# Kernel optimization log

Measured on AMD Instinct MI355X. Metric: run time of the kernel, lower is better.

The kernel has to match this reference:

```python
import jax, jax.numpy as jnp
import numpy as np


def silu(x):
    return x * jax.nn.sigmoid(x)


def setup_inputs() -> dict:
    key = jax.random.key(0)
    ks = jax.random.split(key, 9)
    d_model, d_inner, d_state, d_conv, dt_rank = 1024, 2048, 16, 4, 64
    B, L = 2, 1024
    s = 0.02  # weight init scale for numerical sanity
    return {
        "hidden_states": jax.random.normal(ks[0], (B, L, d_model), jnp.float32),
        "in_proj_w": jax.random.normal(ks[1], (2 * d_inner, d_model), jnp.float32) * s,
        "conv_w": jax.random.normal(ks[2], (d_inner, 1, d_conv), jnp.float32) * 0.2,
        "conv_b": jax.random.normal(ks[3], (d_inner,), jnp.float32) * 0.1,
        "x_proj_w": jax.random.normal(ks[4], (dt_rank + 2 * d_state, d_inner), jnp.float32) * s,
        "dt_proj_w": jax.random.normal(ks[5], (d_inner, dt_rank), jnp.float32) * (dt_rank ** -0.5),
        "dt_proj_b": jax.random.normal(ks[6], (d_inner,), jnp.float32) - 4.0,  # small dt like real init
        "A_log": jnp.log(jnp.tile(jnp.arange(1.0, d_state + 1.0, dtype=jnp.float32)[None, :], (d_inner, 1))),
        "D": jnp.ones((d_inner,), jnp.float32),
        "out_proj_w": jax.random.normal(ks[7], (d_model, d_inner), jnp.float32) * s,
    }


def reference(hidden_states, in_proj_w, conv_w, conv_b, x_proj_w,
              dt_proj_w, dt_proj_b, A_log, D, out_proj_w):
    Bsz, L, _ = hidden_states.shape
    d_inner, d_state = A_log.shape
    dt_rank = dt_proj_w.shape[1]
    K = conv_w.shape[-1]

    xz = jnp.einsum('bld,ed->ble', hidden_states, in_proj_w)  # (B,L,2*di)
    x, z = xz[..., :d_inner], xz[..., d_inner:]

    # causal depthwise conv1d (torch pads K-1 both sides then trims to L)
    xp = jnp.pad(x, ((0, 0), (K - 1, 0), (0, 0)))  # left-pad (B, L+K-1, di)
    w = conv_w[:, 0, :]  # (di, K)
    x = sum(xp[:, k:k + L, :] * w[:, k] for k in range(K)) + conv_b
    x = silu(x)

    x_dbl = jnp.einsum('bld,ed->ble', x, x_proj_w)  # (B,L,dt_rank+2n)
    dt = x_dbl[..., :dt_rank]
    Bm = x_dbl[..., dt_rank:dt_rank + d_state]
    Cm = x_dbl[..., dt_rank + d_state:]
    dt = jax.nn.softplus(jnp.einsum('blr,dr->bld', dt, dt_proj_w) + dt_proj_b)

    A = -jnp.exp(A_log)  # (di, n)
    deltaA = jnp.exp(jnp.einsum('bld,dn->bldn', dt, A))        # (B,L,di,n)
    deltaB_u = jnp.einsum('bld,bln,bld->bldn', dt, Bm, x)      # (B,L,di,n)

    def step(h, inp):
        dA_t, dBu_t, c_t = inp                # (B,di,n),(B,di,n),(B,n)
        h = dA_t * h + dBu_t
        y_t = jnp.einsum('bdn,bn->bd', h, c_t)
        return h, y_t

    h0 = jnp.zeros((Bsz, d_inner, d_state), deltaA.dtype)
    _, ys = jax.lax.scan(step, h0, (deltaA.transpose(1, 0, 2, 3),
                                    deltaB_u.transpose(1, 0, 2, 3),
                                    Cm.transpose(1, 0, 2)))
    y = ys.transpose(1, 0, 2) + x * D        # (B,L,di)
    y = y * silu(z)
    return jnp.einsum('bld,ed->ble', y, out_proj_w)
```

## Files before the change

kernel.cpp:

```cpp
#include <hip/hip_runtime.h>

typedef unsigned short u16;
typedef unsigned int   u32;
typedef __attribute__((ext_vector_type(8))) short bf16x8;
typedef __attribute__((ext_vector_type(4))) float f32x4;

__device__ inline float bf2f(u16 u) { return __uint_as_float(((u32)u) << 16); }
__device__ inline u16 f2bf(float f) {
  u32 u = __float_as_uint(f);
  return (u16)((u + 0x7FFFu + ((u >> 16) & 1u)) >> 16);
}

__device__ inline void gld_lds16(const u16* g, u16* l) {
  __builtin_amdgcn_global_load_lds((const __attribute__((address_space(1))) void*)g,
                                   (__attribute__((address_space(3))) void*)l,
                                   16, 0, 0);
}

__global__ __launch_bounds__(256) void cvt_k(
    const float* __restrict__ hs, const float* __restrict__ w_in,
    const float* __restrict__ w_x, const float* __restrict__ w_dt,
    const float* __restrict__ w_out,
    u16* __restrict__ hs_b, u16* __restrict__ w_in_b, u16* __restrict__ w_x_b,
    u16* __restrict__ w_dt_b, u16* __restrict__ w_out_b)
{
  u32 v = blockIdx.x * 256 + threadIdx.x;
  const float* s; u16* d; u32 loc;
  if      (v < 524288u)  { s = hs;    d = hs_b;    loc = v; }
  else if (v < 1572864u) { s = w_in;  d = w_in_b;  loc = v - 524288u; }
  else if (v < 1622016u) { s = w_x;   d = w_x_b;   loc = v - 1572864u; }
  else if (v < 1654784u) { s = w_dt;  d = w_dt_b;  loc = v - 1622016u; }
  else                   { s = w_out; d = w_out_b; loc = v - 1654784u; }
  float4 f = ((const float4*)s)[loc];
  ushort4 o;
  o.x = f2bf(f.x); o.y = f2bf(f.y); o.z = f2bf(f.z); o.w = f2bf(f.w);
  ((ushort4*)d)[loc] = o;
}

template <int EPI>
__global__ __launch_bounds__(256) void gemm_bt(
    const u16* __restrict__ A, int lda,
    const u16* __restrict__ B, int ldb,
    void* __restrict__ C, int ldc,
    int M, int N, int K,
    const float* __restrict__ bias)
{
  __shared__ u16 sA[128 * 32];
  __shared__ u16 sB[128 * 32];
  const int tid  = threadIdx.x;
  const int wave = tid >> 6, lane = tid & 63;
  const int row0 = blockIdx.x * 128, col0 = blockIdx.y * 128;
  const int r  = lane >> 2, c8 = (lane & 3) * 8;
  const int wm = (wave >> 1) * 64, wn = (wave & 1) * 64;
  const int tm = lane & 15, quad = lane >> 4;

  f32x4 acc[4][4];
#pragma unroll
  for (int i = 0; i < 4; ++i)
#pragma unroll
    for (int j = 0; j < 4; ++j) acc[i][j] = f32x4{0.f, 0.f, 0.f, 0.f};

  for (int k0 = 0; k0 < K; k0 += 32) {
    for (int s = wave; s < 8; s += 4) {
      const u16* ga = A + (size_t)(row0 + s * 16 + r) * lda + (k0 + c8);
      gld_lds16(ga, &sA[s * 512 + lane * 8]);
      int br = col0 + s * 16 + r; br = br < N ? br : N - 1;
      const u16* gb = B + (size_t)br * ldb + (k0 + c8);
      gld_lds16(gb, &sB[s * 512 + lane * 8]);
    }
    __syncthreads();
    bf16x8 af[4], bfv[4];
#pragma unroll
    for (int i = 0; i < 4; ++i) af[i]  = *(const bf16x8*)&sA[(wm + i * 16 + tm) * 32 + quad * 8];
#pragma unroll
    for (int j = 0; j < 4; ++j) bfv[j] = *(const bf16x8*)&sB[(wn + j * 16 + tm) * 32 + quad * 8];
#pragma unroll
    for (int i = 0; i < 4; ++i)
#pragma unroll
      for (int j = 0; j < 4; ++j)
        acc[i][j] = __builtin_amdgcn_mfma_f32_16x16x32_bf16(af[i], bfv[j], acc[i][j], 0, 0, 0);
    __syncthreads();
  }

#pragma unroll
  for (int j = 0; j < 4; ++j) {
    int col = col0 + wn + j * 16 + tm;
    if (col >= N) continue;
#pragma unroll
    for (int i = 0; i < 4; ++i) {
      int rb = row0 + wm + i * 16 + quad * 4;
      f32x4 v = acc[i][j];
#pragma unroll
      for (int t = 0; t < 4; ++t) {
        float f = v[t];
        size_t idx = (size_t)(rb + t) * ldc + col;
        if (EPI == 1) {
          f += bias[col];
          f = (f > 20.f) ? f : log1pf(__expf(f));
          ((float*)C)[idx] = f;
        } else if (EPI == 2) {
          ((float*)C)[idx] = f;
        } else {
          ((u16*)C)[idx] = f2bf(f);
        }
      }
    }
  }
}

__global__ __launch_bounds__(256) void conv_silu_k(
    const u16* __restrict__ xz, const float* __restrict__ cw,
    const float* __restrict__ cb, u16* __restrict__ xc)
{
  int gid = blockIdx.x * 256 + threadIdx.x;
  int d = gid & 2047;
  int row = gid >> 11;
  int l = row & 1023;
  float acc = cb[d];
#pragma unroll
  for (int k = 0; k < 4; ++k) {
    int ll = l - 3 + k;
    if (ll >= 0)
      acc += bf2f(xz[(size_t)(row - 3 + k) * 4096 + d]) * cw[d * 4 + k];
  }
  float s = acc / (1.f + __expf(-acc));
  xc[(size_t)row * 2048 + d] = f2bf(s);
}

#define SSEG 32
#define TSEG 32

__global__ __launch_bounds__(256) void scan1_k(
    const float* __restrict__ dtf,
    const u16* __restrict__ xdbl,
    const u16* __restrict__ xc,
    const float* __restrict__ A_log,
    float* __restrict__ hseg,
    float* __restrict__ sdt_o)
{
  const int L = 1024, DI = 2048;
  int d = blockIdx.x * 256 + threadIdx.x;
  int b = blockIdx.y, s = blockIdx.z;
  float cA[16], h[16];
#pragma unroll
  for (int n = 0; n < 16; ++n) { cA[n] = -__expf(A_log[d * 16 + n]); h[n] = 0.f; }
  float sdt = 0.f;
  size_t row = (size_t)b * L + s * TSEG;
  const float* pdt = dtf + row * DI + d;
  const u16*   px  = xc  + row * DI + d;
  const u16*   pB  = xdbl + row * 96 + 64;
  for (int t = 0; t < TSEG; ++t) {
    float dt = *pdt;
    float xv = bf2f(*px);
    bf16x8 Bv0 = *(const bf16x8*)(pB);
    bf16x8 Bv1 = *(const bf16x8*)(pB + 8);
    float dBu = dt * xv;
    sdt += dt;
#pragma unroll
    for (int n = 0; n < 16; ++n) {
      float dA = __expf(dt * cA[n]);
      float Bn = bf2f((u16)(n < 8 ? Bv0[n] : Bv1[n - 8]));
      h[n] = fmaf(dA, h[n], dBu * Bn);
    }
    pdt += DI; px += DI; pB += 96;
  }
  size_t o = (((size_t)s * 2 + b) * 2048 + d) * 16;
#pragma unroll
  for (int n = 0; n < 16; ++n) hseg[o + n] = h[n];
  sdt_o[((size_t)s * 2 + b) * 2048 + d] = sdt;
}

__global__ __launch_bounds__(256) void combine_k(
    float* hseg, const float* __restrict__ sdt,
    const float* __restrict__ A_log)
{
  int gid = blockIdx.x * 256 + threadIdx.x;
  int b = gid >> 15, d = (gid >> 4) & 2047, n = gid & 15;
  float cA = -__expf(A_log[d * 16 + n]);
  float carry = 0.f;
  for (int s = 0; s < SSEG; ++s) {
    size_t o = (size_t)s * 65536 + gid;
    float he = hseg[o];
    float P = __expf(cA * sdt[(size_t)s * 4096 + b * 2048 + d]);
    hseg[o] = carry;
    carry = fmaf(P, carry, he);
  }
}

__global__ __launch_bounds__(256) void scan3_k(
    const float* __restrict__ dtf,
    const u16* __restrict__ xdbl,
    u16* xcy,
    const u16* __restrict__ xz,
    const float* __restrict__ A_log,
    const float* __restrict__ Dw,
    const float* __restrict__ hstart)
{
  const int L = 1024, DI = 2048;
  int d = blockIdx.x * 256 + threadIdx.x;
  int b = blockIdx.y, s = blockIdx.z;
  float cA[16], h[16];
  size_t ho = (((size_t)s * 2 + b) * 2048 + d) * 16;
#pragma unroll
  for (int n = 0; n < 16; ++n) { cA[n] = -__expf(A_log[d * 16 + n]); h[n] = hstart[ho + n]; }
  float Dd = Dw[d];
  size_t row = (size_t)b * L + s * TSEG;
  const float* pdt = dtf + row * DI + d;
  u16*         px  = xcy + row * DI + d;
  const u16*   pz  = xz  + row * 4096 + 2048 + d;
  const u16*   pBC = xdbl + row * 96 + 64;
  for (int t = 0; t < TSEG; ++t) {
    float dt = *pdt;
    float xv = bf2f(*px);
    float zv = bf2f(*pz);
    bf16x8 Bv0 = *(const bf16x8*)(pBC);
    bf16x8 Bv1 = *(const bf16x8*)(pBC + 8);
    bf16x8 Cv0 = *(const bf16x8*)(pBC + 16);
    bf16x8 Cv1 = *(const bf16x8*)(pBC + 24);
    float dBu = dt * xv;
    float y = xv * Dd;
#pragma unroll
    for (int n = 0; n < 16; ++n) {
      float dA = __expf(dt * cA[n]);
      float Bn = bf2f((u16)(n < 8 ? Bv0[n] : Bv1[n - 8]));
      float Cn = bf2f((u16)(n < 8 ? Cv0[n] : Cv1[n - 8]));
      h[n] = fmaf(dA, h[n], dBu * Bn);
      y = fmaf(h[n], Cn, y);
    }
    float sig = 1.f / (1.f + __expf(-zv));
    *px = f2bf(y * (zv * sig));
    pdt += DI; px += DI; pz += 4096; pBC += 96;
  }
}

extern "C" void kernel_launch(void* const* d_in, const int* in_sizes, int n_in,
                              void* d_out, int out_size, void* d_ws, size_t ws_size,
                              hipStream_t stream)
{
  const float* hs    = (const float*)d_in[0];
  const float* w_in  = (const float*)d_in[1];
  const float* cw    = (const float*)d_in[2];
  const float* cb    = (const float*)d_in[3];
  const float* w_x   = (const float*)d_in[4];
  const float* w_dt  = (const float*)d_in[5];
  const float* b_dt  = (const float*)d_in[6];
  const float* A_log = (const float*)d_in[7];
  const float* Dw    = (const float*)d_in[8];
  const float* w_out = (const float*)d_in[9];

  char* p = (char*)d_ws;
  char* regionA = p;        p += (size_t)12 * 1024 * 1024;
  u16*   w_x_b  = (u16*)p;  p += (size_t)196608 * 2;
  u16*   w_dt_b = (u16*)p;  p += (size_t)131072 * 2;
  u16*   w_out_b= (u16*)p;  p += (size_t)2097152 * 2;
  u16*   xz     = (u16*)p;  p += (size_t)2048 * 4096 * 2;
  u16*   xc     = (u16*)p;  p += (size_t)2048 * 2048 * 2;
  u16*   xdbl   = (u16*)p;  p += (size_t)2048 * 96 * 2;
  float* dtf    = (float*)p;

  u16*   hs_b   = (u16*)regionA;
  u16*   w_in_b = (u16*)(regionA + (size_t)2097152 * 2);
  float* hseg   = (float*)regionA;
  float* sdt    = (float*)(regionA + (size_t)SSEG * 65536 * 4);
  float* out    = (float*)d_out;

  cvt_k<<<8512, 256, 0, stream>>>(hs, w_in, w_x, w_dt, w_out,
                                  hs_b, w_in_b, w_x_b, w_dt_b, w_out_b);
  gemm_bt<0><<<dim3(16, 32), 256, 0, stream>>>(hs_b, 1024, w_in_b, 1024, xz, 4096, 2048, 4096, 1024, nullptr);
  conv_silu_k<<<16384, 256, 0, stream>>>(xz, cw, cb, xc);
  gemm_bt<0><<<dim3(16, 1), 256, 0, stream>>>(xc, 2048, w_x_b, 2048, xdbl, 96, 2048, 96, 2048, nullptr);
  gemm_bt<1><<<dim3(16, 16), 256, 0, stream>>>(xdbl, 96, w_dt_b, 64, dtf, 2048, 2048, 2048, 64, b_dt);
  scan1_k<<<dim3(8, 2, SSEG), 256, 0, stream>>>(dtf, xdbl, xc, A_log, hseg, sdt);
  combine_k<<<256, 256, 0, stream>>>(hseg, sdt, A_log);
  scan3_k<<<dim3(8, 2, SSEG), 256, 0, stream>>>(dtf, xdbl, xc, xz, A_log, Dw, hseg);
  gemm_bt<2><<<dim3(16, 8), 256, 0, stream>>>(xc, 2048, w_out_b, 2048, out, 1024, 2048, 1024, 2048, nullptr);
}
```

Measured before the change: 299.0 us.

## Split-K the x_proj and out_proj GEMMs with a separate reduction kernel

```diff
diff --git a/kernel.cpp b/kernel.cpp
--- a/kernel.cpp
+++ b/kernel.cpp
@@ -42,7 +42,7 @@
     const u16* __restrict__ A, int lda,
     const u16* __restrict__ B, int ldb,
     void* __restrict__ C, int ldc,
-    int M, int N, int K,
+    int M, int N, int Klen,
     const float* __restrict__ bias)
 {
   __shared__ u16 sA[128 * 32];
@@ -50,6 +50,7 @@
   const int tid  = threadIdx.x;
   const int wave = tid >> 6, lane = tid & 63;
   const int row0 = blockIdx.x * 128, col0 = blockIdx.y * 128;
+  const int kbase = blockIdx.z * Klen;
   const int r  = lane >> 2, c8 = (lane & 3) * 8;
   const int wm = (wave >> 1) * 64, wn = (wave & 1) * 64;
   const int tm = lane & 15, quad = lane >> 4;
@@ -60,7 +61,7 @@
 #pragma unroll
     for (int j = 0; j < 4; ++j) acc[i][j] = f32x4{0.f, 0.f, 0.f, 0.f};
 
-  for (int k0 = 0; k0 < K; k0 += 32) {
+  for (int k0 = kbase; k0 < kbase + Klen; k0 += 32) {
     for (int s = wave; s < 8; s += 4) {
       const u16* ga = A + (size_t)(row0 + s * 16 + r) * lda + (k0 + c8);
       gld_lds16(ga, &sA[s * 512 + lane * 8]);
@@ -82,6 +83,7 @@
     __syncthreads();
   }
 
+  const size_t zoff = (size_t)blockIdx.z * M * ldc;
 #pragma unroll
   for (int j = 0; j < 4; ++j) {
     int col = col0 + wn + j * 16 + tm;
@@ -100,11 +102,29 @@
           ((float*)C)[idx] = f;
         } else if (EPI == 2) {
           ((float*)C)[idx] = f;
+        } else if (EPI == 3) {
+          ((float*)C)[zoff + idx] = f;
         } else {
           ((u16*)C)[idx] = f2bf(f);
         }
       }
     }
+  }
+}
+
+template <int OUTBF>
+__global__ __launch_bounds__(256) void red_k(
+    const float* __restrict__ part, void* __restrict__ out, int total, int KS)
+{
+  int i = blockIdx.x * 256 + threadIdx.x;
+  f32x4 a = ((const f32x4*)part)[i];
+  for (int ks = 1; ks < KS; ++ks)
+    a += ((const f32x4*)(part + (size_t)ks * total))[i];
+  if (OUTBF) {
+    ushort4 o; o.x = f2bf(a[0]); o.y = f2bf(a[1]); o.z = f2bf(a[2]); o.w = f2bf(a[3]);
+    ((ushort4*)out)[i] = o;
+  } else {
+    ((f32x4*)out)[i] = a;
   }
 }
 
@@ -256,7 +276,9 @@
   u16*   xz     = (u16*)p;  p += (size_t)2048 * 4096 * 2;
   u16*   xc     = (u16*)p;  p += (size_t)2048 * 2048 * 2;
   u16*   xdbl   = (u16*)p;  p += (size_t)2048 * 96 * 2;
-  float* dtf    = (float*)p;
+  float* dtf    = (float*)p;p += (size_t)2048 * 2048 * 4;
+  float* pout   = (float*)p;p += (size_t)4 * 2048 * 1024 * 4;
+  float* px     = (float*)p;
 
   u16*   hs_b   = (u16*)regionA;
   u16*   w_in_b = (u16*)(regionA + (size_t)2097152 * 2);
@@ -266,12 +288,14 @@
 
   cvt_k<<<8512, 256, 0, stream>>>(hs, w_in, w_x, w_dt, w_out,
                                   hs_b, w_in_b, w_x_b, w_dt_b, w_out_b);
-  gemm_bt<0><<<dim3(16, 32), 256, 0, stream>>>(hs_b, 1024, w_in_b, 1024, xz, 4096, 2048, 4096, 1024, nullptr);
+  gemm_bt<0><<<dim3(16, 32, 1), 256, 0, stream>>>(hs_b, 1024, w_in_b, 1024, xz, 4096, 2048, 4096, 1024, nullptr);
   conv_silu_k<<<16384, 256, 0, stream>>>(xz, cw, cb, xc);
-  gemm_bt<0><<<dim3(16, 1), 256, 0, stream>>>(xc, 2048, w_x_b, 2048, xdbl, 96, 2048, 96, 2048, nullptr);
-  gemm_bt<1><<<dim3(16, 16), 256, 0, stream>>>(xdbl, 96, w_dt_b, 64, dtf, 2048, 2048, 2048, 64, b_dt);
+  gemm_bt<3><<<dim3(16, 1, 16), 256, 0, stream>>>(xc, 2048, w_x_b, 2048, px, 96, 2048, 96, 128, nullptr);
+  red_k<1><<<192, 256, 0, stream>>>(px, xdbl, 196608, 16);
+  gemm_bt<1><<<dim3(16, 16, 1), 256, 0, stream>>>(xdbl, 96, w_dt_b, 64, dtf, 2048, 2048, 2048, 64, b_dt);
   scan1_k<<<dim3(8, 2, SSEG), 256, 0, stream>>>(dtf, xdbl, xc, A_log, hseg, sdt);
   combine_k<<<256, 256, 0, stream>>>(hseg, sdt, A_log);
   scan3_k<<<dim3(8, 2, SSEG), 256, 0, stream>>>(dtf, xdbl, xc, xz, A_log, Dw, hseg);
-  gemm_bt<2><<<dim3(16, 8), 256, 0, stream>>>(xc, 2048, w_out_b, 2048, out, 1024, 2048, 1024, 2048, nullptr);
-}
+  gemm_bt<3><<<dim3(16, 8, 4), 256, 0, stream>>>(xc, 2048, w_out_b, 2048, pout, 1024, 2048, 1024, 512, nullptr);
+  red_k<0><<<2048, 256, 0, stream>>>(pout, out, 2097152, 4);
+}
```

New measurement: 259.6 us. -13.2%, faster.
